# Kernel tuning notes

Hardware: AMD Instinct MI355X
Metric: run time of the kernel (lower is better)

## Reference

```python
import jax, jax.numpy as jnp
import numpy as np

B, N, FIN, FOUT, H = 4, 1024, 256, 256, 8
HID = FOUT // H
ALPHA = 0.2  # LeakyReLU negative slope
NEG = -1e10  # mask fill value (matches -10000000000.0)


def setup_inputs() -> dict:
    key = jax.random.key(0)
    k1, k2, k3, k4, k5 = jax.random.split(key, 5)
    h = jax.random.normal(k1, (B, N, FIN), dtype=jnp.float32)
    adj = jax.random.randint(k2, (B, N, N), 0, 2, dtype=jnp.int32)
    W = jax.random.normal(k3, (FIN, H * HID), dtype=jnp.float32) * 0.05
    a = jax.random.normal(k4, (2 * HID,), dtype=jnp.float32) * 0.05
    bias = jax.random.normal(k5, (FOUT,), dtype=jnp.float32) * 0.05
    return {"h": h, "adj": adj, "W": W, "a": a, "bias": bias}


def reference(h, adj, W, a, bias):
    b, n = h.shape[0], h.shape[1]
    hid = W.shape[1] // H
    s = (h @ W).reshape(b, n, H, hid)  # [B,N,H,F]
    # attention(cat(s_i, s_j)) == s_i @ a_left + s_j @ a_right
    a_left, a_right = a[:hid], a[hid:]
    e_i = jnp.einsum('bnhf,f->bnh', s, a_left)   # [B,N,H]
    e_j = jnp.einsum('bnhf,f->bnh', s, a_right)  # [B,N,H]
    e = e_i[:, :, None, :] + e_j[:, None, :, :]  # [B,i,j,H]
    e = jnp.where(e > 0, e, ALPHA * e)           # LeakyReLU(0.2)
    masked = jnp.where(adj[..., None] == 0, NEG, e)
    # NOTE: original applies softmax over dim=1 (the i axis), then contracts over j
    att = jax.nn.softmax(masked, axis=1)
    # dropout omitted (eval mode / deterministic reference)
    h_prime = jnp.einsum('bijh,bjhf->bihf', att, s)
    out = h_prime.reshape(b, n, H * hid) + bias
    return out
```

## Files before the change

kernel.cpp:

```cpp
#include <hip/hip_runtime.h>
#include <hip/hip_bf16.h>

constexpr int Bb  = 4;
constexpr int Nn  = 1024;
constexpr int Fin = 256;
constexpr int Cc  = 256;
constexpr int Hh  = 8;
constexpr int Hid = 32;
constexpr float Alpha = 0.2f;
constexpr float L2E = 1.4426950408889634f;
constexpr int NCHUNK = 16;

typedef __attribute__((ext_vector_type(8))) short bf16x8;
typedef __attribute__((ext_vector_type(4))) float f32x4;

__device__ __forceinline__ unsigned cvt_pk_bf16(float lo, float hi) {
    unsigned r;
    asm("v_cvt_pk_bf16_f32 %0, %1, %2" : "=v"(r) : "v"(lo), "v"(hi));
    return r;
}

__global__ __launch_bounds__(256) void k_gemm(const float* __restrict__ hin,
                                              const float* __restrict__ W,
                                              const float* __restrict__ av,
                                              float* __restrict__ eiT,
                                              float* __restrict__ ejT,
                                              unsigned short* __restrict__ sC) {
    __shared__ unsigned short Asm[64 * 256];
    __shared__ unsigned short Bsm[64 * 256];
    const int t = threadIdx.x;
    const int hp = blockIdx.x;
    const int rt = blockIdx.y;
    const int b = rt >> 4;
    const int row0m = (rt & 15) * 64;
    const int grow0 = rt * 64;
    const int col0 = hp * 64;

    #pragma unroll
    for (int i = 0; i < 16; ++i) {
        int fi = i * 256 + t;
        int r = fi >> 6, c4 = fi & 63;
        float4 v = *reinterpret_cast<const float4*>(&hin[(size_t)(grow0 + r) * Fin + c4 * 4]);
        uint2 pk = make_uint2(cvt_pk_bf16(v.x, v.y), cvt_pk_bf16(v.z, v.w));
        *reinterpret_cast<uint2*>(reinterpret_cast<char*>(Asm) + r * 512 +
            (((c4 >> 1) ^ ((r >> 1) & 7)) << 4) + ((c4 & 1) << 3)) = pk;
    }
    #pragma unroll
    for (int i = 0; i < 32; ++i) {
        int p = i * 256 + t;
        int c = p & 63, k = (p >> 6) << 1;
        float w0 = W[(size_t)k * Cc + col0 + c];
        float w1 = W[(size_t)(k + 1) * Cc + col0 + c];
        unsigned pk = cvt_pk_bf16(w0, w1);
        *reinterpret_cast<unsigned*>(reinterpret_cast<char*>(Bsm) + c * 512 +
            (((k >> 3) ^ ((c >> 1) & 7)) << 4) + ((k & 7) << 1)) = pk;
    }
    __syncthreads();

    const int w = t >> 6, l = t & 63;
    const int lr = l & 15, lg = l >> 4;
    const int ar = w * 16 + lr;
    f32x4 acc[4] = {{0.f,0.f,0.f,0.f},{0.f,0.f,0.f,0.f},{0.f,0.f,0.f,0.f},{0.f,0.f,0.f,0.f}};

    #pragma unroll
    for (int ks = 0; ks < 8; ++ks) {
        bf16x8 af = *reinterpret_cast<const bf16x8*>(reinterpret_cast<char*>(Asm) +
            ar * 512 + ((((ks << 2) + lg) ^ ((ar >> 1) & 7)) << 4));
        #pragma unroll
        for (int n = 0; n < 4; ++n) {
            int c = n * 16 + lr;
            bf16x8 bf = *reinterpret_cast<const bf16x8*>(reinterpret_cast<char*>(Bsm) +
                c * 512 + ((((ks << 2) + lg) ^ ((c >> 1) & 7)) << 4));
            acc[n] = __builtin_amdgcn_mfma_f32_16x16x32_bf16(af, bf, acc[n], 0, 0, 0);
        }
    }

    const int jt16 = (row0m >> 4) + w;
    #pragma unroll
    for (int n = 0; n < 4; ++n) {
        int bh = b * 8 + hp * 2 + (n >> 1);
        uint2 pk = make_uint2(cvt_pk_bf16(acc[n][0], acc[n][1]),
                              cvt_pk_bf16(acc[n][2], acc[n][3]));
        *reinterpret_cast<uint2*>(reinterpret_cast<char*>(sC) +
            ((((size_t)bh * 64 + jt16) * 2 + (n & 1)) * 64 + l) * 8) = pk;
    }

    float aL0 = av[lr], aL1 = av[16 + lr], aR0 = av[32 + lr], aR1 = av[48 + lr];
    #pragma unroll
    for (int hh = 0; hh < 2; ++hh) {
        float pi[4], pj[4];
        #pragma unroll
        for (int reg = 0; reg < 4; ++reg) {
            pi[reg] = acc[hh * 2][reg] * aL0 + acc[hh * 2 + 1][reg] * aL1;
            pj[reg] = acc[hh * 2][reg] * aR0 + acc[hh * 2 + 1][reg] * aR1;
        }
        #pragma unroll
        for (int m = 1; m < 16; m <<= 1) {
            #pragma unroll
            for (int reg = 0; reg < 4; ++reg) {
                pi[reg] += __shfl_xor(pi[reg], m);
                pj[reg] += __shfl_xor(pj[reg], m);
            }
        }
        if (lr == 0) {
            int bh = b * 8 + hp * 2 + hh;
            #pragma unroll
            for (int reg = 0; reg < 4; ++reg) {
                int row = row0m + w * 16 + lg * 4 + reg;
                eiT[bh * Nn + row] = pi[reg] * L2E;
                ejT[bh * Nn + row] = pj[reg] * L2E;
            }
        }
    }
}

__global__ __launch_bounds__(256) void k_colsum(const float* __restrict__ eiT,
                                                const float* __restrict__ ejT,
                                                const int* __restrict__ adj,
                                                float* __restrict__ Zp,
                                                unsigned long long* __restrict__ adjBT) {
    const int ic = blockIdx.x;
    const int jt = blockIdx.y;
    const int b  = blockIdx.z;
    const int i0 = ic * 64;
    const int j0 = jt * 64;
    const int t = threadIdx.x;
    const int jj = t & 63;
    const int g = t >> 6;
    __shared__ float eis[64 * Hh];
    __shared__ float red[4 * 64 * Hh];
    for (int v = t; v < 64 * Hh; v += 256) {
        int h = v >> 6, i = v & 63;
        eis[i * Hh + h] = eiT[((size_t)b * Hh + h) * Nn + i0 + i];
    }
    float ejr[Hh];
    #pragma unroll
    for (int hh = 0; hh < Hh; ++hh)
        ejr[hh] = ejT[((size_t)b * Hh + hh) * Nn + j0 + jj];
    __syncthreads();
    float z[Hh] = {};
    const int* ap = &adj[((size_t)b * Nn + i0 + g * 16) * Nn + j0 + jj];
    #pragma unroll 4
    for (int ii = 0; ii < 16; ++ii) {
        int a = ap[(size_t)ii * Nn];
        unsigned long long bal = __ballot(a != 0);
        if (jj == 0)
            adjBT[((size_t)b * 16 + jt) * Nn + (i0 + g * 16 + ii)] = bal;
        float mf = (float)(a != 0);
        const float* ep = &eis[(g * 16 + ii) * Hh];
        #pragma unroll
        for (int hh = 0; hh < Hh; ++hh) {
            float x = ep[hh] + ejr[hh];
            x = fmaxf(x, Alpha * x);
            z[hh] = fmaf(mf, exp2f(x), z[hh]);
        }
    }
    #pragma unroll
    for (int hh = 0; hh < Hh; ++hh)
        red[(g * 64 + jj) * Hh + hh] = z[hh];
    __syncthreads();
    for (int v = t; v < 64 * Hh; v += 256) {
        float sum = red[v] + red[512 + v] + red[1024 + v] + red[1536 + v];
        Zp[(size_t)ic * (Bb * Nn * Hh) + ((size_t)b * Nn + j0) * Hh + v] = sum;
    }
}

__global__ void k_ezrT(const float* __restrict__ Zp, const float* __restrict__ ejT,
                       float2* __restrict__ ezrT) {
    const int tid = blockIdx.x * 256 + threadIdx.x;
    const int n = tid & 1023;
    const int bh = tid >> 10;
    const int b = bh >> 3, h = bh & 7;
    const int src = (b * Nn + n) * Hh + h;
    constexpr int S = Bb * Nn * Hh;
    float sum = 0.f;
    #pragma unroll
    for (int c = 0; c < NCHUNK; ++c) sum += Zp[(size_t)c * S + src];
    ezrT[tid] = make_float2(ejT[tid], 1.0f / sum);
}

__global__ __launch_bounds__(256) void k_agg(const unsigned short* __restrict__ sC,
                                             const float* __restrict__ eiT,
                                             const float2* __restrict__ ezrT,
                                             const unsigned long long* __restrict__ adjBT,
                                             const float* __restrict__ bias,
                                             float* __restrict__ out) {
    const int bid = blockIdx.x;
    const int xcd = bid & 7, g = bid >> 3;
    const int bh = xcd * 4 + (g & 3);
    const int it = g >> 2;
    const int b = bh >> 3, h = bh & 7;
    const int t = threadIdx.x, w = t >> 6, l = t & 63;
    const int lg = l >> 4;
    const int row = it * 64 + w * 16 + (l & 15);
    const float ei_r = eiT[bh * Nn + row];

    const float4* ez4 = reinterpret_cast<const float4*>(ezrT + (size_t)bh * Nn);
    const unsigned long long* scp =
        reinterpret_cast<const unsigned long long*>(sC) + (size_t)bh * 8192;
    const int lpos = ((l >> 4) & 1) * 32 + (l & 15);

    f32x4 acc0 = {0.f, 0.f, 0.f, 0.f}, acc1 = {0.f, 0.f, 0.f, 0.f};

    for (int jk = 0; jk < 32; ++jk) {
        const int j8 = jk * 32 + lg * 8;
        float4 za = ez4[(j8 >> 1) + 0];
        float4 zb = ez4[(j8 >> 1) + 1];
        float4 zc = ez4[(j8 >> 1) + 2];
        float4 zd = ez4[(j8 >> 1) + 3];
        unsigned long long m64 = adjBT[((size_t)b * 16 + (jk >> 1)) * Nn + row];
        unsigned mb = (unsigned)(m64 >> ((jk & 1) * 32 + lg * 8)) & 0xFFu;

        float wv[8];
        {
            float ejv[8] = {za.x, za.z, zb.x, zb.z, zc.x, zc.z, zd.x, zd.z};
            float rzv[8] = {za.y, za.w, zb.y, zb.w, zc.y, zc.w, zd.y, zd.w};
            #pragma unroll
            for (int e = 0; e < 8; ++e) {
                float x = ei_r + ejv[e];
                x = fmaxf(x, Alpha * x);
                float ww = exp2f(x) * rzv[e];
                wv[e] = ((mb >> e) & 1u) ? ww : 0.0f;
            }
        }
        union { bf16x8 v; unsigned u[4]; } A;
        A.u[0] = cvt_pk_bf16(wv[0], wv[1]);
        A.u[1] = cvt_pk_bf16(wv[2], wv[3]);
        A.u[2] = cvt_pk_bf16(wv[4], wv[5]);
        A.u[3] = cvt_pk_bf16(wv[6], wv[7]);

        const int j16 = jk * 2 + (l >> 5);
        union { bf16x8 v; unsigned long long q[2]; } B0, B1;
        const unsigned long long* p0 = scp + ((size_t)j16 * 2 + 0) * 64 + lpos;
        const unsigned long long* p1 = scp + ((size_t)j16 * 2 + 1) * 64 + lpos;
        B0.q[0] = p0[0];  B0.q[1] = p0[16];
        B1.q[0] = p1[0];  B1.q[1] = p1[16];

        acc0 = __builtin_amdgcn_mfma_f32_16x16x32_bf16(A.v, B0.v, acc0, 0, 0, 0);
        acc1 = __builtin_amdgcn_mfma_f32_16x16x32_bf16(A.v, B1.v, acc1, 0, 0, 0);
    }

    const int col = l & 15;
    const float bv0 = bias[h * Hid + col];
    const float bv1 = bias[h * Hid + 16 + col];
    const int r0 = it * 64 + w * 16 + lg * 4;
    #pragma unroll
    for (int reg = 0; reg < 4; ++reg) {
        float* op = &out[((size_t)b * Nn + r0 + reg) * Cc + h * Hid];
        op[col]      = acc0[reg] + bv0;
        op[16 + col] = acc1[reg] + bv1;
    }
}

extern "C" void kernel_launch(void* const* d_in, const int* in_sizes, int n_in,
                              void* d_out, int out_size, void* d_ws, size_t ws_size,
                              hipStream_t stream) {
    const float* hin  = (const float*)d_in[0];
    const int*   adj  = (const int*)d_in[1];
    const float* W    = (const float*)d_in[2];
    const float* a    = (const float*)d_in[3];
    const float* bias = (const float*)d_in[4];
    float* out = (float*)d_out;
    float* ws  = (float*)d_ws;

    float*  eiT  = ws;
    float*  ejT  = ws + 32768;
    float*  Zp   = ws + 65536;
    float2* ezrT = (float2*)(ws + 589824);
    unsigned long long* adjBT = (unsigned long long*)(ws + 655360);
    unsigned short* sC = (unsigned short*)(ws + 786432);

    k_gemm  <<<dim3(4, 64),                 256, 0, stream>>>(hin, W, a, eiT, ejT, sC);
    k_colsum<<<dim3(16, 16, 4),             256, 0, stream>>>(eiT, ejT, adj, Zp, adjBT);
    k_ezrT  <<<dim3((Bb * Nn * Hh) / 256),  256, 0, stream>>>(Zp, ejT, ezrT);
    k_agg   <<<dim3(512),                   256, 0, stream>>>(sC, eiT, ezrT, adjBT, bias, out);
}
```

Measured before the change: 115.3 us.

## Pretranspose W with folded attention columns; fuse Z reduction into aggregation

Adds a small pre-kernel that transposes W to bf16 once and folds the attention vectors into 16 extra columns (W·a_left, W·a_right scaled by log2e). The GEMM then reads B fragments straight from global memory and computes ei/ej with an extra MFMA column block instead of shuffle reductions. The separate ezrT kernel is removed: Zp is written in a transposed layout and each aggregation block sums the partials into shared memory itself. The intent is to cut redundant W conversion and one launch, at the cost of an extra launch, per-block recomputation of the Z reduction, and bf16 rounding of the folded attention weights.

```diff
diff --git a/kernel.cpp b/kernel.cpp
--- a/kernel.cpp
+++ b/kernel.cpp
@@ -20,21 +20,59 @@
     return r;
 }
 
+__global__ __launch_bounds__(256) void k_wext(const float* __restrict__ W,
+                                              const float* __restrict__ av,
+                                              unsigned short* __restrict__ WT) {
+    const int t = threadIdx.x;
+    const int k0 = blockIdx.y * 32;
+    if (blockIdx.x < 8) {
+        __shared__ float tile[32][33];
+        const int c0 = blockIdx.x * 32;
+        {
+            int kk = t >> 3, c4 = t & 7;
+            float4 v = *reinterpret_cast<const float4*>(&W[(size_t)(k0 + kk) * Cc + c0 + c4 * 4]);
+            tile[kk][c4 * 4 + 0] = v.x;
+            tile[kk][c4 * 4 + 1] = v.y;
+            tile[kk][c4 * 4 + 2] = v.z;
+            tile[kk][c4 * 4 + 3] = v.w;
+        }
+        __syncthreads();
+        int cc = t & 31, kq = t >> 5;
+        float f0 = tile[kq * 4 + 0][cc], f1 = tile[kq * 4 + 1][cc];
+        float f2 = tile[kq * 4 + 2][cc], f3 = tile[kq * 4 + 3][cc];
+        uint2 pk = make_uint2(cvt_pk_bf16(f0, f1), cvt_pk_bf16(f2, f3));
+        *reinterpret_cast<uint2*>(reinterpret_cast<char*>(WT) +
+            (size_t)(c0 + cc) * 512 + (k0 + kq * 4) * 2) = pk;
+    } else {
+        int kk = t >> 3, c = t & 7;
+        const float* wrow = &W[(size_t)(k0 + kk) * Cc + c * 32];
+        float dl = 0.f, dr = 0.f;
+        #pragma unroll
+        for (int q = 0; q < 8; ++q) {
+            float4 wv = *reinterpret_cast<const float4*>(&wrow[q * 4]);
+            float4 al = *reinterpret_cast<const float4*>(&av[q * 4]);
+            float4 ar = *reinterpret_cast<const float4*>(&av[32 + q * 4]);
+            dl += wv.x * al.x + wv.y * al.y + wv.z * al.z + wv.w * al.w;
+            dr += wv.x * ar.x + wv.y * ar.y + wv.z * ar.z + wv.w * ar.w;
+        }
+        dl *= L2E; dr *= L2E;
+        WT[(size_t)(256 + c) * 256 + k0 + kk] = (unsigned short)(cvt_pk_bf16(dl, dl) & 0xFFFFu);
+        WT[(size_t)(264 + c) * 256 + k0 + kk] = (unsigned short)(cvt_pk_bf16(dr, dr) & 0xFFFFu);
+    }
+}
+
 __global__ __launch_bounds__(256) void k_gemm(const float* __restrict__ hin,
-                                              const float* __restrict__ W,
-                                              const float* __restrict__ av,
+                                              const unsigned short* __restrict__ WT,
                                               float* __restrict__ eiT,
                                               float* __restrict__ ejT,
                                               unsigned short* __restrict__ sC) {
     __shared__ unsigned short Asm[64 * 256];
-    __shared__ unsigned short Bsm[64 * 256];
     const int t = threadIdx.x;
     const int hp = blockIdx.x;
     const int rt = blockIdx.y;
     const int b = rt >> 4;
     const int row0m = (rt & 15) * 64;
     const int grow0 = rt * 64;
-    const int col0 = hp * 64;
 
     #pragma unroll
     for (int i = 0; i < 16; ++i) {
@@ -45,71 +83,53 @@
         *reinterpret_cast<uint2*>(reinterpret_cast<char*>(Asm) + r * 512 +
             (((c4 >> 1) ^ ((r >> 1) & 7)) << 4) + ((c4 & 1) << 3)) = pk;
     }
-    #pragma unroll
-    for (int i = 0; i < 32; ++i) {
-        int p = i * 256 + t;
-        int c = p & 63, k = (p >> 6) << 1;
-        float w0 = W[(size_t)k * Cc + col0 + c];
-        float w1 = W[(size_t)(k + 1) * Cc + col0 + c];
-        unsigned pk = cvt_pk_bf16(w0, w1);
-        *reinterpret_cast<unsigned*>(reinterpret_cast<char*>(Bsm) + c * 512 +
-            (((k >> 3) ^ ((c >> 1) & 7)) << 4) + ((k & 7) << 1)) = pk;
-    }
     __syncthreads();
 
     const int w = t >> 6, l = t & 63;
     const int lr = l & 15, lg = l >> 4;
     const int ar = w * 16 + lr;
-    f32x4 acc[4] = {{0.f,0.f,0.f,0.f},{0.f,0.f,0.f,0.f},{0.f,0.f,0.f,0.f},{0.f,0.f,0.f,0.f}};
-
-    #pragma unroll
-    for (int ks = 0; ks < 8; ++ks) {
-        bf16x8 af = *reinterpret_cast<const bf16x8*>(reinterpret_cast<char*>(Asm) +
-            ar * 512 + ((((ks << 2) + lg) ^ ((ar >> 1) & 7)) << 4));
+
+    if (hp < 4) {
+        f32x4 acc[4] = {{0.f,0.f,0.f,0.f},{0.f,0.f,0.f,0.f},{0.f,0.f,0.f,0.f},{0.f,0.f,0.f,0.f}};
+        #pragma unroll
+        for (int ks = 0; ks < 8; ++ks) {
+            bf16x8 af = *reinterpret_cast<const bf16x8*>(reinterpret_cast<char*>(Asm) +
+                ar * 512 + ((((ks << 2) + lg) ^ ((ar >> 1) & 7)) << 4));
+            #pragma unroll
+            for (int n = 0; n < 4; ++n) {
+                bf16x8 bf = *reinterpret_cast<const bf16x8*>(
+                    &WT[(size_t)(hp * 64 + n * 16 + lr) * 256 + ks * 32 + lg * 8]);
+                acc[n] = __builtin_amdgcn_mfma_f32_16x16x32_bf16(af, bf, acc[n], 0, 0, 0);
+            }
+        }
+        const int jt16 = (row0m >> 4) + w;
         #pragma unroll
         for (int n = 0; n < 4; ++n) {
-            int c = n * 16 + lr;
-            bf16x8 bf = *reinterpret_cast<const bf16x8*>(reinterpret_cast<char*>(Bsm) +
-                c * 512 + ((((ks << 2) + lg) ^ ((c >> 1) & 7)) << 4));
-            acc[n] = __builtin_amdgcn_mfma_f32_16x16x32_bf16(af, bf, acc[n], 0, 0, 0);
-        }
-    }
-
-    const int jt16 = (row0m >> 4) + w;
-    #pragma unroll
-    for (int n = 0; n < 4; ++n) {
-        int bh = b * 8 + hp * 2 + (n >> 1);
-        uint2 pk = make_uint2(cvt_pk_bf16(acc[n][0], acc[n][1]),
-                              cvt_pk_bf16(acc[n][2], acc[n][3]));
-        *reinterpret_cast<uint2*>(reinterpret_cast<char*>(sC) +
-            ((((size_t)bh * 64 + jt16) * 2 + (n & 1)) * 64 + l) * 8) = pk;
-    }
-
-    float aL0 = av[lr], aL1 = av[16 + lr], aR0 = av[32 + lr], aR1 = av[48 + lr];
-    #pragma unroll
-    for (int hh = 0; hh < 2; ++hh) {
-        float pi[4], pj[4];
-        #pragma unroll
-        for (int reg = 0; reg < 4; ++reg) {
-            pi[reg] = acc[hh * 2][reg] * aL0 + acc[hh * 2 + 1][reg] * aL1;
-            pj[reg] = acc[hh * 2][reg] * aR0 + acc[hh * 2 + 1][reg] * aR1;
-        }
-        #pragma unroll
-        for (int m = 1; m < 16; m <<= 1) {
-            #pragma unroll
-            for (int reg = 0; reg < 4; ++reg) {
-                pi[reg] += __shfl_xor(pi[reg], m);
-                pj[reg] += __shfl_xor(pj[reg], m);
-            }
-        }
-        if (lr == 0) {
-            int bh = b * 8 + hp * 2 + hh;
-            #pragma unroll
-            for (int reg = 0; reg < 4; ++reg) {
-                int row = row0m + w * 16 + lg * 4 + reg;
-                eiT[bh * Nn + row] = pi[reg] * L2E;
-                ejT[bh * Nn + row] = pj[reg] * L2E;
-            }
+            int bh = b * 8 + hp * 2 + (n >> 1);
+            uint2 pk = make_uint2(cvt_pk_bf16(acc[n][0], acc[n][1]),
+                                  cvt_pk_bf16(acc[n][2], acc[n][3]));
+            *reinterpret_cast<uint2*>(reinterpret_cast<char*>(sC) +
+                ((((size_t)bh * 64 + jt16) * 2 + (n & 1)) * 64 + l) * 8) = pk;
+        }
+    } else {
+        f32x4 acc = {0.f, 0.f, 0.f, 0.f};
+        #pragma unroll
+        for (int ks = 0; ks < 8; ++ks) {
+            bf16x8 af = *reinterpret_cast<const bf16x8*>(reinterpret_cast<char*>(Asm) +
+                ar * 512 + ((((ks << 2) + lg) ^ ((ar >> 1) & 7)) << 4));
+            bf16x8 bf = *reinterpret_cast<const bf16x8*>(
+                &WT[(size_t)(256 + lr) * 256 + ks * 32 + lg * 8]);
+            acc = __builtin_amdgcn_mfma_f32_16x16x32_bf16(af, bf, acc, 0, 0, 0);
+        }
+        const int rowg = row0m + w * 16 + lg * 4;
+        if (lr < 8) {
+            #pragma unroll
+            for (int reg = 0; reg < 4; ++reg)
+                eiT[(size_t)(b * 8 + lr) * Nn + rowg + reg] = acc[reg];
+        } else {
+            #pragma unroll
+            for (int reg = 0; reg < 4; ++reg)
+                ejT[(size_t)(b * 8 + lr - 8) * Nn + rowg + reg] = acc[reg];
         }
     }
 }
@@ -160,28 +180,17 @@
         red[(g * 64 + jj) * Hh + hh] = z[hh];
     __syncthreads();
     for (int v = t; v < 64 * Hh; v += 256) {
-        float sum = red[v] + red[512 + v] + red[1024 + v] + red[1536 + v];
-        Zp[(size_t)ic * (Bb * Nn * Hh) + ((size_t)b * Nn + j0) * Hh + v] = sum;
-    }
-}
-
-__global__ void k_ezrT(const float* __restrict__ Zp, const float* __restrict__ ejT,
-                       float2* __restrict__ ezrT) {
-    const int tid = blockIdx.x * 256 + threadIdx.x;
-    const int n = tid & 1023;
-    const int bh = tid >> 10;
-    const int b = bh >> 3, h = bh & 7;
-    const int src = (b * Nn + n) * Hh + h;
-    constexpr int S = Bb * Nn * Hh;
-    float sum = 0.f;
-    #pragma unroll
-    for (int c = 0; c < NCHUNK; ++c) sum += Zp[(size_t)c * S + src];
-    ezrT[tid] = make_float2(ejT[tid], 1.0f / sum);
+        int h2 = v >> 6, jj2 = v & 63;
+        float sum = red[jj2 * Hh + h2] + red[(64 + jj2) * Hh + h2] +
+                    red[(128 + jj2) * Hh + h2] + red[(192 + jj2) * Hh + h2];
+        Zp[(size_t)ic * (Bb * Nn * Hh) + ((size_t)b * Hh + h2) * Nn + j0 + jj2] = sum;
+    }
 }
 
 __global__ __launch_bounds__(256) void k_agg(const unsigned short* __restrict__ sC,
                                              const float* __restrict__ eiT,
-                                             const float2* __restrict__ ezrT,
+                                             const float* __restrict__ ejT,
+                                             const float* __restrict__ Zp,
                                              const unsigned long long* __restrict__ adjBT,
                                              const float* __restrict__ bias,
                                              float* __restrict__ out) {
@@ -193,9 +202,21 @@
     const int t = threadIdx.x, w = t >> 6, l = t & 63;
     const int lg = l >> 4;
     const int row = it * 64 + w * 16 + (l & 15);
-    const float ei_r = eiT[bh * Nn + row];
-
-    const float4* ez4 = reinterpret_cast<const float4*>(ezrT + (size_t)bh * Nn);
+
+    __shared__ __align__(16) float2 ez_s[Nn];
+    #pragma unroll
+    for (int q = 0; q < 4; ++q) {
+        int j = q * 256 + t;
+        float sum = 0.f;
+        #pragma unroll
+        for (int c = 0; c < NCHUNK; ++c)
+            sum += Zp[(size_t)c * (Bb * Nn * Hh) + (size_t)bh * Nn + j];
+        ez_s[j] = make_float2(ejT[(size_t)bh * Nn + j], 1.0f / sum);
+    }
+    __syncthreads();
+
+    const float ei_r = eiT[(size_t)bh * Nn + row];
+    const float4* ez4 = reinterpret_cast<const float4*>(ez_s);
     const unsigned long long* scp =
         reinterpret_cast<const unsigned long long*>(sC) + (size_t)bh * 8192;
     const int lpos = ((l >> 4) & 1) * 32 + (l & 15);
@@ -263,15 +284,15 @@
     float* out = (float*)d_out;
     float* ws  = (float*)d_ws;
 
-    float*  eiT  = ws;
-    float*  ejT  = ws + 32768;
-    float*  Zp   = ws + 65536;
-    float2* ezrT = (float2*)(ws + 589824);
-    unsigned long long* adjBT = (unsigned long long*)(ws + 655360);
-    unsigned short* sC = (unsigned short*)(ws + 786432);
-
-    k_gemm  <<<dim3(4, 64),                 256, 0, stream>>>(hin, W, a, eiT, ejT, sC);
-    k_colsum<<<dim3(16, 16, 4),             256, 0, stream>>>(eiT, ejT, adj, Zp, adjBT);
-    k_ezrT  <<<dim3((Bb * Nn * Hh) / 256),  256, 0, stream>>>(Zp, ejT, ezrT);
-    k_agg   <<<dim3(512),                   256, 0, stream>>>(sC, eiT, ezrT, adjBT, bias, out);
-}
+    float* eiT = ws;
+    float* ejT = ws + 32768;
+    float* Zp  = ws + 65536;
+    unsigned short* WT = (unsigned short*)(ws + 589824);
+    unsigned long long* adjBT = (unsigned long long*)(ws + 624640);
+    unsigned short* sC = (unsigned short*)(ws + 755712);
+
+    k_wext  <<<dim3(9, 8),       256, 0, stream>>>(W, a, WT);
+    k_gemm  <<<dim3(5, 64),      256, 0, stream>>>(hin, WT, eiT, ejT, sC);
+    k_colsum<<<dim3(16, 16, 4),  256, 0, stream>>>(eiT, ejT, adj, Zp, adjBT);
+    k_agg   <<<dim3(512),        256, 0, stream>>>(sC, eiT, ejT, Zp, adjBT, bias, out);
+}
```

Result: slower. 117.7 us (+2.0%).

## Fuse colsum, normalization and aggregation into one kernel with grid barrier

Applied to the files above, without the earlier changes.

Merges the column-sum, reciprocal-normalizer and aggregation kernels into a single persistent kernel of 512 blocks. Each block does two colsum units, then waits on a global atomic barrier. After the barrier each block reduces the partial sums for its head into shared memory instead of reading a precomputed ezrT buffer. Zp is now written in a head-major layout to match. This removes two kernel launches and the ezrT round trip through global memory. In exchange it relies on all 512 blocks being co-resident (launch bounds of 2 blocks per CU), needs an extra memset per call, and repeats the Zp reduction across the row-tile blocks that share a head.

```diff
diff --git a/kernel.cpp b/kernel.cpp
--- a/kernel.cpp
+++ b/kernel.cpp
@@ -10,6 +10,7 @@
 constexpr float Alpha = 0.2f;
 constexpr float L2E = 1.4426950408889634f;
 constexpr int NCHUNK = 16;
+constexpr unsigned NBLK2 = 512;
 
 typedef __attribute__((ext_vector_type(8))) short bf16x8;
 typedef __attribute__((ext_vector_type(4))) float f32x4;
@@ -114,88 +115,99 @@
     }
 }
 
-__global__ __launch_bounds__(256) void k_colsum(const float* __restrict__ eiT,
-                                                const float* __restrict__ ejT,
-                                                const int* __restrict__ adj,
-                                                float* __restrict__ Zp,
-                                                unsigned long long* __restrict__ adjBT) {
-    const int ic = blockIdx.x;
-    const int jt = blockIdx.y;
-    const int b  = blockIdx.z;
-    const int i0 = ic * 64;
-    const int j0 = jt * 64;
-    const int t = threadIdx.x;
-    const int jj = t & 63;
-    const int g = t >> 6;
+__global__ __launch_bounds__(256, 2) void k_fused(const float* __restrict__ eiT,
+                                                  const float* __restrict__ ejT,
+                                                  const int* __restrict__ adj,
+                                                  const unsigned short* __restrict__ sC,
+                                                  const float* __restrict__ bias,
+                                                  float* __restrict__ Zp,
+                                                  unsigned long long* __restrict__ adjBT,
+                                                  unsigned* __restrict__ bar,
+                                                  float* __restrict__ out) {
     __shared__ float eis[64 * Hh];
     __shared__ float red[4 * 64 * Hh];
-    for (int v = t; v < 64 * Hh; v += 256) {
-        int h = v >> 6, i = v & 63;
-        eis[i * Hh + h] = eiT[((size_t)b * Hh + h) * Nn + i0 + i];
-    }
-    float ejr[Hh];
-    #pragma unroll
-    for (int hh = 0; hh < Hh; ++hh)
-        ejr[hh] = ejT[((size_t)b * Hh + hh) * Nn + j0 + jj];
-    __syncthreads();
-    float z[Hh] = {};
-    const int* ap = &adj[((size_t)b * Nn + i0 + g * 16) * Nn + j0 + jj];
-    #pragma unroll 4
-    for (int ii = 0; ii < 16; ++ii) {
-        int a = ap[(size_t)ii * Nn];
-        unsigned long long bal = __ballot(a != 0);
-        if (jj == 0)
-            adjBT[((size_t)b * 16 + jt) * Nn + (i0 + g * 16 + ii)] = bal;
-        float mf = (float)(a != 0);
-        const float* ep = &eis[(g * 16 + ii) * Hh];
-        #pragma unroll
-        for (int hh = 0; hh < Hh; ++hh) {
-            float x = ep[hh] + ejr[hh];
-            x = fmaxf(x, Alpha * x);
-            z[hh] = fmaf(mf, exp2f(x), z[hh]);
-        }
-    }
-    #pragma unroll
-    for (int hh = 0; hh < Hh; ++hh)
-        red[(g * 64 + jj) * Hh + hh] = z[hh];
-    __syncthreads();
-    for (int v = t; v < 64 * Hh; v += 256) {
-        float sum = red[v] + red[512 + v] + red[1024 + v] + red[1536 + v];
-        Zp[(size_t)ic * (Bb * Nn * Hh) + ((size_t)b * Nn + j0) * Hh + v] = sum;
-    }
-}
-
-__global__ void k_ezrT(const float* __restrict__ Zp, const float* __restrict__ ejT,
-                       float2* __restrict__ ezrT) {
-    const int tid = blockIdx.x * 256 + threadIdx.x;
-    const int n = tid & 1023;
-    const int bh = tid >> 10;
+    __shared__ __align__(16) float2 ez_s[Nn];
+    const int t = threadIdx.x;
+    const int bid = blockIdx.x;
+
+    #pragma unroll
+    for (int q = 0; q < 2; ++q) {
+        const int unit = (bid << 1) | q;
+        const int ic = unit & 15;
+        const int jt = (unit >> 4) & 15;
+        const int b  = unit >> 8;
+        const int i0 = ic * 64;
+        const int j0 = jt * 64;
+        const int jj = t & 63;
+        const int g = t >> 6;
+        __syncthreads();
+        for (int v = t; v < 64 * Hh; v += 256) {
+            int h = v >> 6, i = v & 63;
+            eis[i * Hh + h] = eiT[((size_t)b * Hh + h) * Nn + i0 + i];
+        }
+        float ejr[Hh];
+        #pragma unroll
+        for (int hh = 0; hh < Hh; ++hh)
+            ejr[hh] = ejT[((size_t)b * Hh + hh) * Nn + j0 + jj];
+        __syncthreads();
+        float z[Hh] = {};
+        const int* ap = &adj[((size_t)b * Nn + i0 + g * 16) * Nn + j0 + jj];
+        #pragma unroll 8
+        for (int ii = 0; ii < 16; ++ii) {
+            int a = ap[(size_t)ii * Nn];
+            unsigned long long bal = __ballot(a != 0);
+            if (jj == 0)
+                adjBT[((size_t)b * 16 + jt) * Nn + (i0 + g * 16 + ii)] = bal;
+            float mf = (float)(a != 0);
+            const float* ep = &eis[(g * 16 + ii) * Hh];
+            #pragma unroll
+            for (int hh = 0; hh < Hh; ++hh) {
+                float x = ep[hh] + ejr[hh];
+                x = fmaxf(x, Alpha * x);
+                z[hh] = fmaf(mf, exp2f(x), z[hh]);
+            }
+        }
+        #pragma unroll
+        for (int hh = 0; hh < Hh; ++hh)
+            red[(g * 64 + jj) * Hh + hh] = z[hh];
+        __syncthreads();
+        for (int v = t; v < 64 * Hh; v += 256) {
+            int h2 = v >> 6, jj2 = v & 63;
+            float sum = red[jj2 * Hh + h2] + red[(64 + jj2) * Hh + h2] +
+                        red[(128 + jj2) * Hh + h2] + red[(192 + jj2) * Hh + h2];
+            Zp[(size_t)ic * (Bb * Nn * Hh) + ((size_t)b * Hh + h2) * Nn + j0 + jj2] = sum;
+        }
+    }
+
+    __syncthreads();
+    if (t == 0) {
+        __hip_atomic_fetch_add(bar, 1u, __ATOMIC_RELEASE, __HIP_MEMORY_SCOPE_AGENT);
+        while (__hip_atomic_load(bar, __ATOMIC_ACQUIRE, __HIP_MEMORY_SCOPE_AGENT) < NBLK2)
+            __builtin_amdgcn_s_sleep(2);
+    }
+    __syncthreads();
+
+    const int xcd = bid & 7, g2 = bid >> 3;
+    const int bh = xcd * 4 + (g2 & 3);
+    const int it = g2 >> 2;
     const int b = bh >> 3, h = bh & 7;
-    const int src = (b * Nn + n) * Hh + h;
-    constexpr int S = Bb * Nn * Hh;
-    float sum = 0.f;
-    #pragma unroll
-    for (int c = 0; c < NCHUNK; ++c) sum += Zp[(size_t)c * S + src];
-    ezrT[tid] = make_float2(ejT[tid], 1.0f / sum);
-}
-
-__global__ __launch_bounds__(256) void k_agg(const unsigned short* __restrict__ sC,
-                                             const float* __restrict__ eiT,
-                                             const float2* __restrict__ ezrT,
-                                             const unsigned long long* __restrict__ adjBT,
-                                             const float* __restrict__ bias,
-                                             float* __restrict__ out) {
-    const int bid = blockIdx.x;
-    const int xcd = bid & 7, g = bid >> 3;
-    const int bh = xcd * 4 + (g & 3);
-    const int it = g >> 2;
-    const int b = bh >> 3, h = bh & 7;
-    const int t = threadIdx.x, w = t >> 6, l = t & 63;
+    const int w = t >> 6, l = t & 63;
     const int lg = l >> 4;
     const int row = it * 64 + w * 16 + (l & 15);
-    const float ei_r = eiT[bh * Nn + row];
-
-    const float4* ez4 = reinterpret_cast<const float4*>(ezrT + (size_t)bh * Nn);
+
+    #pragma unroll
+    for (int q = 0; q < 4; ++q) {
+        int j = q * 256 + t;
+        float sum = 0.f;
+        #pragma unroll
+        for (int c = 0; c < NCHUNK; ++c)
+            sum += Zp[(size_t)c * (Bb * Nn * Hh) + (size_t)bh * Nn + j];
+        ez_s[j] = make_float2(ejT[(size_t)bh * Nn + j], 1.0f / sum);
+    }
+    __syncthreads();
+
+    const float ei_r = eiT[(size_t)bh * Nn + row];
+    const float4* ez4 = reinterpret_cast<const float4*>(ez_s);
     const unsigned long long* scp =
         reinterpret_cast<const unsigned long long*>(sC) + (size_t)bh * 8192;
     const int lpos = ((l >> 4) & 1) * 32 + (l & 15);
@@ -263,15 +275,15 @@
     float* out = (float*)d_out;
     float* ws  = (float*)d_ws;
 
-    float*  eiT  = ws;
-    float*  ejT  = ws + 32768;
-    float*  Zp   = ws + 65536;
-    float2* ezrT = (float2*)(ws + 589824);
-    unsigned long long* adjBT = (unsigned long long*)(ws + 655360);
-    unsigned short* sC = (unsigned short*)(ws + 786432);
-
-    k_gemm  <<<dim3(4, 64),                 256, 0, stream>>>(hin, W, a, eiT, ejT, sC);
-    k_colsum<<<dim3(16, 16, 4),             256, 0, stream>>>(eiT, ejT, adj, Zp, adjBT);
-    k_ezrT  <<<dim3((Bb * Nn * Hh) / 256),  256, 0, stream>>>(Zp, ejT, ezrT);
-    k_agg   <<<dim3(512),                   256, 0, stream>>>(sC, eiT, ezrT, adjBT, bias, out);
-}
+    float* eiT = ws;
+    float* ejT = ws + 32768;
+    float* Zp  = ws + 65536;
+    unsigned long long* adjBT = (unsigned long long*)(ws + 589824);
+    unsigned short* sC = (unsigned short*)(ws + 1114112);
+    unsigned* bar = (unsigned*)(ws + 1638400);
+
+    hipMemsetAsync(bar, 0, sizeof(unsigned), stream);
+    k_gemm <<<dim3(4, 64), 256, 0, stream>>>(hin, W, a, eiT, ejT, sC);
+    k_fused<<<dim3(NBLK2), 256, 0, stream>>>(eiT, ejT, adj, sC, bias,
+                                             Zp, adjBT, bar, out);
+}
```

Measured after the change: 145.8 us. +26.4%, slower.
